# Kernel optimization log

Hardware: AMD Instinct MI355X
Metric: run time of the kernel (lower is better)

## Reference

```python
import jax, jax.numpy as jnp
import numpy as np

N_NODES = 100000
K_NBRS = 16
N_EDGES = N_NODES * K_NBRS


def setup_inputs() -> dict:
    key = jax.random.key(0)
    ks = jax.random.split(key, 20)
    x = jax.random.normal(ks[0], (N_NODES, 3), dtype=jnp.float32)
    # knn-like edge list: every node is the target of exactly K_NBRS edges
    dst = jnp.repeat(jnp.arange(N_NODES, dtype=jnp.int64), K_NBRS)
    src = jax.random.randint(ks[1], (N_EDGES,), 0, N_NODES, dtype=jnp.int64)
    edge_index = jnp.stack([src, dst], axis=0)  # [2, E], row0=source(j), row1=target(i)

    def lin_init(k, fan_in, fan_out):
        s = 1.0 / np.sqrt(fan_in)
        return jax.random.uniform(k, (fan_in, fan_out), jnp.float32, -s, s)

    inp = {"x": x, "edge_index": edge_index}
    inp["W1"], inp["b1"] = lin_init(ks[2], 6, 64), jnp.zeros((64,), jnp.float32)
    for i, kk in zip(range(2, 6), ks[3:7]):
        inp[f"W{i}"] = lin_init(kk, 128, 64)
        inp[f"b{i}"] = jnp.zeros((64,), jnp.float32)
    inp["Wa"], inp["ba"] = lin_init(ks[8], 128, 128), jnp.zeros((128,), jnp.float32)
    inp["Wb"], inp["bb"] = lin_init(ks[9], 128, 3), jnp.zeros((3,), jnp.float32)
    return inp


def edge_conv(x, src, dst, W, b):
    # PyG EdgeConv: message = nn(cat([x_i, x_j - x_i])), max-aggregate at target i
    xi = x[dst]                      # [E, C] center (target) features
    xj = x[src]                      # [E, C] neighbor (source) features
    msg = jnp.concatenate([xi, xj - xi], axis=-1)  # [E, 2C]
    msg = jax.nn.relu(msg @ W + b)                 # [E, 64] per-edge MLP
    return jax.ops.segment_max(msg, dst, num_segments=N_NODES)  # [N, 64]


def reference(x, edge_index, W1, b1, W2, b2, W3, b3, W4, b4, W5, b5, Wa, ba, Wb, bb):
    src, dst = edge_index[0], edge_index[1]
    h = edge_conv(x, src, dst, W1, b1)
    h = edge_conv(h, src, dst, W2, b2)
    h = edge_conv(h, src, dst, W3, b3)
    h = edge_conv(h, src, dst, W4, b4)
    h = edge_conv(h, src, dst, W5, b5)           # [N, 64]
    g = jnp.max(h, axis=0, keepdims=True)        # [1, 64] global max
    feat = jnp.concatenate([h, jnp.broadcast_to(g, h.shape)], axis=1)  # [N, 128]
    out = jax.nn.relu(feat @ Wa + ba) @ Wb + bb  # [N, 3]
    return x + out
```

## Files before the change

kernel.cpp:

```cpp
#include <hip/hip_runtime.h>
#include <math.h>

#define N_NODES 100000
#define K_NBRS 16
#define N_EDGES (N_NODES * K_NBRS)
#define TPB 256
#define NBLK 2048

typedef __attribute__((ext_vector_type(8))) short short8;
typedef __attribute__((ext_vector_type(8))) float float8;
typedef __attribute__((ext_vector_type(4))) float float4_;
typedef __attribute__((ext_vector_type(4))) int int4_;
typedef __attribute__((ext_vector_type(4))) unsigned short ushort4_;

__device__ __forceinline__ unsigned short f2bf(float f) {
  unsigned int u = __float_as_uint(f);
  u += 0x7fffu + ((u >> 16) & 1u);
  return (unsigned short)(u >> 16);
}
__device__ __forceinline__ float bf2f(unsigned short b) {
  return __uint_as_float(((unsigned int)b) << 16);
}

__global__ void k_normsrc(const int* __restrict__ ei, int* __restrict__ srcout) {
  const bool is64 = (ei[1] == 0) && (ei[3] == 0) && (ei[5] == 0) && (ei[7] == 0);
  const int tid = blockIdx.x * blockDim.x + threadIdx.x;
  const int stride = gridDim.x * blockDim.x;
  for (int e = tid; e < N_EDGES; e += stride)
    srcout[e] = is64 ? ei[2 * e] : ei[e];
}

__global__ void k_layer1(const float* __restrict__ x, const float* __restrict__ W1,
                         const float* __restrict__ b1,
                         float* __restrict__ A, unsigned short* __restrict__ B) {
  const int lane = threadIdx.x & 63;
  const int nwaves = (gridDim.x * blockDim.x) >> 6;
  const int wid0 = (blockIdx.x * blockDim.x + threadIdx.x) >> 6;
  float w[6];
#pragma unroll
  for (int k = 0; k < 6; ++k) w[k] = W1[k * 64 + lane];
  const float bias = b1[lane];
  for (int i0 = wid0; i0 < N_NODES; i0 += nwaves) {
    const int i = __builtin_amdgcn_readfirstlane(i0);
    const float x0 = x[3 * i], x1 = x[3 * i + 1], x2 = x[3 * i + 2];
    const float b = fmaf(x0, w[3], fmaf(x1, w[4], x2 * w[5]));
    const float a = bias + fmaf(x0, w[0] - w[3],
                          fmaf(x1, w[1] - w[4], x2 * (w[2] - w[5])));
    A[(size_t)i * 64 + lane] = a;
    B[(size_t)i * 64 + lane] = f2bf(b);
  }
}

template <bool DO_GMAX>
__global__ void k_aggr(const int* __restrict__ src,
                       const float* __restrict__ Ain,
                       const unsigned short* __restrict__ Bin,
                       unsigned short* __restrict__ hout, float* __restrict__ P) {
  const int lane = threadIdx.x & 63;
  const int q = lane >> 4;
  const int c4 = (lane & 15) * 4;
  const int nw = (gridDim.x * blockDim.x) >> 6;
  const int w0 = (blockIdx.x * blockDim.x + threadIdx.x) >> 6;
  float4_ gmax = (float4_)(0.f);
  for (int p = w0; p * 4 < N_NODES; p += nw) {
    const int i0 = __builtin_amdgcn_readfirstlane(p * 4);
    int4_ idx[4];
#pragma unroll
    for (int n = 0; n < 4; ++n)
      idx[n] = *(const int4_*)(src + (size_t)(i0 + n) * 16 + q * 4);
    ushort4_ gv[4][4];
#pragma unroll
    for (int n = 0; n < 4; ++n)
#pragma unroll
      for (int e = 0; e < 4; ++e)
        gv[n][e] = *(const ushort4_*)(Bin + (size_t)idx[n][e] * 64 + c4);
    const float4_ av = *(const float4_*)(Ain + (size_t)(i0 + q) * 64 + c4);
    float4_ m[4];
#pragma unroll
    for (int n = 0; n < 4; ++n) {
#pragma unroll
      for (int t = 0; t < 4; ++t) {
        const float v0 = bf2f(gv[n][0][t]), v1 = bf2f(gv[n][1][t]);
        const float v2 = bf2f(gv[n][2][t]), v3 = bf2f(gv[n][3][t]);
        m[n][t] = fmaxf(fmaxf(v0, v1), fmaxf(v2, v3));
      }
#pragma unroll
      for (int t = 0; t < 4; ++t) {
        float v = m[n][t];
        v = fmaxf(v, __shfl_xor(v, 16));
        v = fmaxf(v, __shfl_xor(v, 32));
        m[n][t] = v;
      }
    }
    ushort4_ hb;
#pragma unroll
    for (int t = 0; t < 4; ++t) {
      float v = m[0][t];
      v = (q == 1) ? m[1][t] : v;
      v = (q == 2) ? m[2][t] : v;
      v = (q == 3) ? m[3][t] : v;
      const float h = fmaxf(av[t] + v, 0.f);
      hb[t] = f2bf(h);
      if constexpr (DO_GMAX) gmax[t] = fmaxf(gmax[t], h);
    }
    *(ushort4_*)(hout + (size_t)(i0 + q) * 64 + c4) = hb;
  }
  if constexpr (DO_GMAX) {
    __shared__ float red[TPB][4];
#pragma unroll
    for (int t = 0; t < 4; ++t) red[threadIdx.x][t] = gmax[t];
    __syncthreads();
    if (threadIdx.x < 64) {
      const int c = threadIdx.x, j = c >> 2, t = c & 3;
      float mm = 0.f;
#pragma unroll
      for (int w = 0; w < 4; ++w)
#pragma unroll
        for (int qq = 0; qq < 4; ++qq)
          mm = fmaxf(mm, red[w * 64 + qq * 16 + j][t]);
      P[(size_t)blockIdx.x * 64 + c] = mm;
    }
  }
}

__global__ __launch_bounds__(TPB, 2)
void k_gemm(const unsigned short* __restrict__ h, const float* __restrict__ W,
            const float* __restrict__ bn,
            float* __restrict__ Aout, unsigned short* __restrict__ Bout) {
  __shared__ unsigned short lwhi[128 * 72];
  __shared__ unsigned short lwlo[128 * 72];
  for (int idx = threadIdx.x; idx < 8192; idx += TPB) {
    const int k = idx >> 7, j = idx & 127;
    const float v = (j < 64) ? (W[k * 64 + j] - W[(64 + k) * 64 + j])
                             : W[(64 + k) * 64 + (j - 64)];
    const unsigned short hi = f2bf(v);
    lwhi[j * 72 + k] = hi;
    lwlo[j * 72 + k] = f2bf(v - bf2f(hi));
  }
  __syncthreads();
  const int lane = threadIdx.x & 63;
  const int wav = threadIdx.x >> 6;
  const int l15 = lane & 15, lg = lane >> 4;
  short8 bhi[8][2], blo[8][2];
#pragma unroll
  for (int ct = 0; ct < 8; ++ct)
#pragma unroll
    for (int kk = 0; kk < 2; ++kk) {
      const int off = (ct * 16 + l15) * 72 + kk * 32 + lg * 8;
      bhi[ct][kk] = *(const short8*)&lwhi[off];
      blo[ct][kk] = *(const short8*)&lwlo[off];
    }
  float bv[4];
#pragma unroll
  for (int ct = 0; ct < 4; ++ct) bv[ct] = bn[ct * 16 + l15];
  const int NT = (N_NODES + 63) / 64;
  for (int t = blockIdx.x; t < NT; t += gridDim.x) {
    const int nb = t * 64 + wav * 16;
    const int row = min(nb + l15, N_NODES - 1);
    const unsigned short* hr = h + (size_t)row * 64;
    float4_ acc[8];
#pragma unroll
    for (int ct = 0; ct < 8; ++ct) acc[ct] = (float4_)(0.f);
#pragma unroll
    for (int kk = 0; kk < 2; ++kk) {
      const short8 ahi = *(const short8*)(hr + kk * 32 + lg * 8);
#pragma unroll
      for (int ct = 0; ct < 8; ++ct) {
        acc[ct] = __builtin_amdgcn_mfma_f32_16x16x32_bf16(ahi, bhi[ct][kk], acc[ct], 0, 0, 0);
        acc[ct] = __builtin_amdgcn_mfma_f32_16x16x32_bf16(ahi, blo[ct][kk], acc[ct], 0, 0, 0);
      }
    }
#pragma unroll
    for (int ct = 0; ct < 8; ++ct)
#pragma unroll
      for (int r = 0; r < 4; ++r) {
        const int node = nb + lg * 4 + r;
        if (node < N_NODES) {
          if (ct < 4)
            Aout[(size_t)node * 64 + ct * 16 + l15] = acc[ct][r] + bv[ct];
          else
            Bout[(size_t)node * 64 + (ct - 4) * 16 + l15] = f2bf(acc[ct][r]);
        }
      }
  }
}

__global__ void k_gred(const float* __restrict__ P, float* __restrict__ g) {
  __shared__ float red[16][64];
  const int lane = threadIdx.x & 63;
  const int w = threadIdx.x >> 6;
  float m = 0.f;
  for (int r = w; r < NBLK; r += 16)
    m = fmaxf(m, P[(size_t)r * 64 + lane]);
  red[w][lane] = m;
  __syncthreads();
  if (threadIdx.x < 64) {
    float mm = 0.f;
#pragma unroll
    for (int k = 0; k < 16; ++k) mm = fmaxf(mm, red[k][lane]);
    g[lane] = mm;
  }
}

__global__ __launch_bounds__(TPB, 2)
void k_final(const unsigned short* __restrict__ h, const float* __restrict__ g,
             const float* __restrict__ Wa, const float* __restrict__ ba,
             const float* __restrict__ Wb, const float* __restrict__ bb,
             const float* __restrict__ x, float* __restrict__ out) {
  __shared__ unsigned short lwhi[128 * 72];
  __shared__ unsigned short lwlo[128 * 72];
  __shared__ float sgt[128];
  for (int idx = threadIdx.x; idx < 8192; idx += TPB) {
    const int k = idx >> 7, j = idx & 127;
    const float v = Wa[k * 128 + j];
    const unsigned short hi = f2bf(v);
    lwhi[j * 72 + k] = hi;
    lwlo[j * 72 + k] = f2bf(v - bf2f(hi));
  }
  if (threadIdx.x < 128) {
    const int c = threadIdx.x;
    float s = ba[c];
    for (int k = 0; k < 64; ++k) s = fmaf(g[k], Wa[(64 + k) * 128 + c], s);
    sgt[c] = s;
  }
  __syncthreads();
  const int lane = threadIdx.x & 63;
  const int wav = threadIdx.x >> 6;
  const int l15 = lane & 15, lg = lane >> 4;
  short8 bhi[8][2], blo[8][2];
#pragma unroll
  for (int ct = 0; ct < 8; ++ct)
#pragma unroll
    for (int kk = 0; kk < 2; ++kk) {
      const int off = (ct * 16 + l15) * 72 + kk * 32 + lg * 8;
      bhi[ct][kk] = *(const short8*)&lwhi[off];
      blo[ct][kk] = *(const short8*)&lwlo[off];
    }
  float gtv[8];
#pragma unroll
  for (int ct = 0; ct < 8; ++ct) gtv[ct] = sgt[ct * 16 + l15];
  float wbv[8][3];
#pragma unroll
  for (int ct = 0; ct < 8; ++ct)
#pragma unroll
    for (int jj = 0; jj < 3; ++jj)
      wbv[ct][jj] = Wb[(ct * 16 + l15) * 3 + jj];
  const float bbl = (l15 == 0) ? bb[0] : (l15 == 1 ? bb[1] : bb[2]);
  const int NT = (N_NODES + 63) / 64;
  for (int t = blockIdx.x; t < NT; t += gridDim.x) {
    const int nb = t * 64 + wav * 16;
    const int row = min(nb + l15, N_NODES - 1);
    const unsigned short* hr = h + (size_t)row * 64;
    float4_ acc[8];
#pragma unroll
    for (int ct = 0; ct < 8; ++ct) acc[ct] = (float4_)(0.f);
#pragma unroll
    for (int kk = 0; kk < 2; ++kk) {
      const short8 ahi = *(const short8*)(hr + kk * 32 + lg * 8);
#pragma unroll
      for (int ct = 0; ct < 8; ++ct) {
        acc[ct] = __builtin_amdgcn_mfma_f32_16x16x32_bf16(ahi, bhi[ct][kk], acc[ct], 0, 0, 0);
        acc[ct] = __builtin_amdgcn_mfma_f32_16x16x32_bf16(ahi, blo[ct][kk], acc[ct], 0, 0, 0);
      }
    }
#pragma unroll
    for (int r = 0; r < 4; ++r) {
      float t0 = 0.f, t1 = 0.f, t2 = 0.f;
#pragma unroll
      for (int ct = 0; ct < 8; ++ct) {
        const float hd = fmaxf(acc[ct][r] + gtv[ct], 0.f);
        t0 = fmaf(hd, wbv[ct][0], t0);
        t1 = fmaf(hd, wbv[ct][1], t1);
        t2 = fmaf(hd, wbv[ct][2], t2);
      }
#pragma unroll
      for (int off = 1; off < 16; off <<= 1) {
        t0 += __shfl_xor(t0, off);
        t1 += __shfl_xor(t1, off);
        t2 += __shfl_xor(t2, off);
      }
      const int node = nb + lg * 4 + r;
      if (node < N_NODES && l15 < 3) {
        const float tj = (l15 == 0) ? t0 : (l15 == 1 ? t1 : t2);
        out[(size_t)node * 3 + l15] = x[(size_t)node * 3 + l15] + tj + bbl;
      }
    }
  }
}

extern "C" void kernel_launch(void* const* d_in, const int* in_sizes, int n_in,
                              void* d_out, int out_size, void* d_ws, size_t ws_size,
                              hipStream_t stream) {
  const float* x  = (const float*)d_in[0];
  const int*   ei = (const int*)d_in[1];
  const float* W1 = (const float*)d_in[2];
  const float* b1 = (const float*)d_in[3];
  const float* W2 = (const float*)d_in[4];
  const float* b2 = (const float*)d_in[5];
  const float* W3 = (const float*)d_in[6];
  const float* b3 = (const float*)d_in[7];
  const float* W4 = (const float*)d_in[8];
  const float* b4 = (const float*)d_in[9];
  const float* W5 = (const float*)d_in[10];
  const float* b5 = (const float*)d_in[11];
  const float* Wa = (const float*)d_in[12];
  const float* ba = (const float*)d_in[13];
  const float* Wb = (const float*)d_in[14];
  const float* bb = (const float*)d_in[15];
  float* out = (float*)d_out;

  float* ws = (float*)d_ws;
  int* srcbuf = (int*)ws;
  float* A0 = ws + 1600000;
  float* A1 = A0 + 6400000;
  unsigned short* H  = (unsigned short*)(A1 + 6400000);
  unsigned short* B0 = H + 6400000;
  unsigned short* B1 = B0 + 6400000;
  float* P = (float*)(B1 + 6400000);
  float* g = P + (size_t)NBLK * 64;

  k_normsrc<<<1024, TPB, 0, stream>>>(ei, srcbuf);
  k_layer1<<<NBLK, TPB, 0, stream>>>(x, W1, b1, A0, B0);
  k_aggr<false><<<NBLK, TPB, 0, stream>>>(srcbuf, A0, B0, H, nullptr);
  k_gemm<<<512, TPB, 0, stream>>>(H, W2, b2, A1, B1);
  k_aggr<false><<<NBLK, TPB, 0, stream>>>(srcbuf, A1, B1, H, nullptr);
  k_gemm<<<512, TPB, 0, stream>>>(H, W3, b3, A0, B0);
  k_aggr<false><<<NBLK, TPB, 0, stream>>>(srcbuf, A0, B0, H, nullptr);
  k_gemm<<<512, TPB, 0, stream>>>(H, W4, b4, A1, B1);
  k_aggr<false><<<NBLK, TPB, 0, stream>>>(srcbuf, A1, B1, H, nullptr);
  k_gemm<<<512, TPB, 0, stream>>>(H, W5, b5, A0, B0);
  k_aggr<true><<<NBLK, TPB, 0, stream>>>(srcbuf, A0, B0, H, P);
  k_gred<<<1, 1024, 0, stream>>>(P, g);
  k_final<<<512, TPB, 0, stream>>>(H, g, Wa, ba, Wb, bb, x, out);
}
```

Before: 378.5 us.

## Store A in bf16, prefetch next indices in aggr, fuse prologue kernels, widen grids

Stores the per-node center term A in bf16 instead of fp32, which halves its write traffic in gemm and its read traffic in aggregation. The aggregation loop is software-pipelined so the next iteration's source indices and A values load while the current gather completes. The edge-index normalisation and layer-1 kernels are merged into one launch, and the gemm and final kernels get twice as many blocks. These gain memory bandwidth and latency hiding but add bf16 rounding to A and raise register pressure in aggregation.

```diff
diff --git a/kernel.cpp b/kernel.cpp
--- a/kernel.cpp
+++ b/kernel.cpp
@@ -8,7 +8,6 @@
 #define NBLK 2048
 
 typedef __attribute__((ext_vector_type(8))) short short8;
-typedef __attribute__((ext_vector_type(8))) float float8;
 typedef __attribute__((ext_vector_type(4))) float float4_;
 typedef __attribute__((ext_vector_type(4))) int int4_;
 typedef __attribute__((ext_vector_type(4))) unsigned short ushort4_;
@@ -22,20 +21,19 @@
   return __uint_as_float(((unsigned int)b) << 16);
 }
 
-__global__ void k_normsrc(const int* __restrict__ ei, int* __restrict__ srcout) {
+__global__ void k_pre(const int* __restrict__ ei, int* __restrict__ srcout,
+                      const float* __restrict__ x, const float* __restrict__ W1,
+                      const float* __restrict__ b1,
+                      unsigned short* __restrict__ A, unsigned short* __restrict__ B) {
   const bool is64 = (ei[1] == 0) && (ei[3] == 0) && (ei[5] == 0) && (ei[7] == 0);
   const int tid = blockIdx.x * blockDim.x + threadIdx.x;
   const int stride = gridDim.x * blockDim.x;
   for (int e = tid; e < N_EDGES; e += stride)
     srcout[e] = is64 ? ei[2 * e] : ei[e];
-}
-
-__global__ void k_layer1(const float* __restrict__ x, const float* __restrict__ W1,
-                         const float* __restrict__ b1,
-                         float* __restrict__ A, unsigned short* __restrict__ B) {
-  const int lane = threadIdx.x & 63;
-  const int nwaves = (gridDim.x * blockDim.x) >> 6;
-  const int wid0 = (blockIdx.x * blockDim.x + threadIdx.x) >> 6;
+
+  const int lane = threadIdx.x & 63;
+  const int nwaves = stride >> 6;
+  const int wid0 = tid >> 6;
   float w[6];
 #pragma unroll
   for (int k = 0; k < 6; ++k) w[k] = W1[k * 64 + lane];
@@ -46,14 +44,14 @@
     const float b = fmaf(x0, w[3], fmaf(x1, w[4], x2 * w[5]));
     const float a = bias + fmaf(x0, w[0] - w[3],
                           fmaf(x1, w[1] - w[4], x2 * (w[2] - w[5])));
-    A[(size_t)i * 64 + lane] = a;
+    A[(size_t)i * 64 + lane] = f2bf(a);
     B[(size_t)i * 64 + lane] = f2bf(b);
   }
 }
 
 template <bool DO_GMAX>
 __global__ void k_aggr(const int* __restrict__ src,
-                       const float* __restrict__ Ain,
+                       const unsigned short* __restrict__ Ain,
                        const unsigned short* __restrict__ Bin,
                        unsigned short* __restrict__ hout, float* __restrict__ P) {
   const int lane = threadIdx.x & 63;
@@ -62,19 +60,34 @@
   const int nw = (gridDim.x * blockDim.x) >> 6;
   const int w0 = (blockIdx.x * blockDim.x + threadIdx.x) >> 6;
   float4_ gmax = (float4_)(0.f);
-  for (int p = w0; p * 4 < N_NODES; p += nw) {
+  int p = w0;
+  int4_ idx[4];
+  ushort4_ avp;
+  if (p * 4 < N_NODES) {
     const int i0 = __builtin_amdgcn_readfirstlane(p * 4);
-    int4_ idx[4];
 #pragma unroll
     for (int n = 0; n < 4; ++n)
       idx[n] = *(const int4_*)(src + (size_t)(i0 + n) * 16 + q * 4);
+    avp = *(const ushort4_*)(Ain + (size_t)(i0 + q) * 64 + c4);
+  }
+  while (p * 4 < N_NODES) {
+    const int i0 = __builtin_amdgcn_readfirstlane(p * 4);
     ushort4_ gv[4][4];
 #pragma unroll
     for (int n = 0; n < 4; ++n)
 #pragma unroll
       for (int e = 0; e < 4; ++e)
         gv[n][e] = *(const ushort4_*)(Bin + (size_t)idx[n][e] * 64 + c4);
-    const float4_ av = *(const float4_*)(Ain + (size_t)(i0 + q) * 64 + c4);
+    const int pn = p + nw;
+    int4_ idxn[4];
+    ushort4_ avn;
+    if (pn * 4 < N_NODES) {
+      const int i1 = __builtin_amdgcn_readfirstlane(pn * 4);
+#pragma unroll
+      for (int n = 0; n < 4; ++n)
+        idxn[n] = *(const int4_*)(src + (size_t)(i1 + n) * 16 + q * 4);
+      avn = *(const ushort4_*)(Ain + (size_t)(i1 + q) * 64 + c4);
+    }
     float4_ m[4];
 #pragma unroll
     for (int n = 0; n < 4; ++n) {
@@ -99,11 +112,15 @@
       v = (q == 1) ? m[1][t] : v;
       v = (q == 2) ? m[2][t] : v;
       v = (q == 3) ? m[3][t] : v;
-      const float h = fmaxf(av[t] + v, 0.f);
+      const float h = fmaxf(bf2f(avp[t]) + v, 0.f);
       hb[t] = f2bf(h);
       if constexpr (DO_GMAX) gmax[t] = fmaxf(gmax[t], h);
     }
     *(ushort4_*)(hout + (size_t)(i0 + q) * 64 + c4) = hb;
+    p = pn;
+#pragma unroll
+    for (int n = 0; n < 4; ++n) idx[n] = idxn[n];
+    avp = avn;
   }
   if constexpr (DO_GMAX) {
     __shared__ float red[TPB][4];
@@ -126,7 +143,7 @@
 __global__ __launch_bounds__(TPB, 2)
 void k_gemm(const unsigned short* __restrict__ h, const float* __restrict__ W,
             const float* __restrict__ bn,
-            float* __restrict__ Aout, unsigned short* __restrict__ Bout) {
+            unsigned short* __restrict__ Aout, unsigned short* __restrict__ Bout) {
   __shared__ unsigned short lwhi[128 * 72];
   __shared__ unsigned short lwlo[128 * 72];
   for (int idx = threadIdx.x; idx < 8192; idx += TPB) {
@@ -177,7 +194,7 @@
         const int node = nb + lg * 4 + r;
         if (node < N_NODES) {
           if (ct < 4)
-            Aout[(size_t)node * 64 + ct * 16 + l15] = acc[ct][r] + bv[ct];
+            Aout[(size_t)node * 64 + ct * 16 + l15] = f2bf(acc[ct][r] + bv[ct]);
           else
             Bout[(size_t)node * 64 + (ct - 4) * 16 + l15] = f2bf(acc[ct][r]);
         }
@@ -311,25 +328,24 @@
 
   float* ws = (float*)d_ws;
   int* srcbuf = (int*)ws;
-  float* A0 = ws + 1600000;
-  float* A1 = A0 + 6400000;
-  unsigned short* H  = (unsigned short*)(A1 + 6400000);
+  unsigned short* A0 = (unsigned short*)(ws + 1600000);
+  unsigned short* A1 = A0 + 6400000;
+  unsigned short* H  = A1 + 6400000;
   unsigned short* B0 = H + 6400000;
   unsigned short* B1 = B0 + 6400000;
   float* P = (float*)(B1 + 6400000);
   float* g = P + (size_t)NBLK * 64;
 
-  k_normsrc<<<1024, TPB, 0, stream>>>(ei, srcbuf);
-  k_layer1<<<NBLK, TPB, 0, stream>>>(x, W1, b1, A0, B0);
+  k_pre<<<NBLK, TPB, 0, stream>>>(ei, srcbuf, x, W1, b1, A0, B0);
   k_aggr<false><<<NBLK, TPB, 0, stream>>>(srcbuf, A0, B0, H, nullptr);
-  k_gemm<<<512, TPB, 0, stream>>>(H, W2, b2, A1, B1);
+  k_gemm<<<1024, TPB, 0, stream>>>(H, W2, b2, A1, B1);
   k_aggr<false><<<NBLK, TPB, 0, stream>>>(srcbuf, A1, B1, H, nullptr);
-  k_gemm<<<512, TPB, 0, stream>>>(H, W3, b3, A0, B0);
+  k_gemm<<<1024, TPB, 0, stream>>>(H, W3, b3, A0, B0);
   k_aggr<false><<<NBLK, TPB, 0, stream>>>(srcbuf, A0, B0, H, nullptr);
-  k_gemm<<<512, TPB, 0, stream>>>(H, W4, b4, A1, B1);
+  k_gemm<<<1024, TPB, 0, stream>>>(H, W4, b4, A1, B1);
   k_aggr<false><<<NBLK, TPB, 0, stream>>>(srcbuf, A1, B1, H, nullptr);
-  k_gemm<<<512, TPB, 0, stream>>>(H, W5, b5, A0, B0);
+  k_gemm<<<1024, TPB, 0, stream>>>(H, W5, b5, A0, B0);
   k_aggr<true><<<NBLK, TPB, 0, stream>>>(srcbuf, A0, B0, H, P);
   k_gred<<<1, 1024, 0, stream>>>(P, g);
-  k_final<<<512, TPB, 0, stream>>>(H, g, Wa, ba, Wb, bb, x, out);
-}
+  k_final<<<1024, TPB, 0, stream>>>(H, g, Wa, ba, Wb, bb, x, out);
+}
```

Result: slower. 400.2 us (+5.7%).
